# Kernel optimization log

Hardware: AMD Instinct MI355X
Metric: run time of the kernel (lower is better)

The kernel has to match this reference:

```python
import jax, jax.numpy as jnp
import numpy as np

N_NODES = 50000
N_EDGES = 800000
D_IN = 128
D_OUT = 128


def setup_inputs() -> dict:
    key = jax.random.key(0)
    k1, k2, k3, k4 = jax.random.split(key, 4)
    feature = jax.random.normal(k1, (N_NODES, D_IN), dtype=jnp.float32)
    edge_src = jax.random.randint(k2, (N_EDGES,), 0, N_NODES, dtype=jnp.int32)
    edge_dst = jax.random.randint(k3, (N_EDGES,), 0, N_NODES, dtype=jnp.int32)
    W = jax.random.normal(k4, (D_IN, D_OUT), dtype=jnp.float32) * (1.0 / np.sqrt(D_IN))
    b = jnp.zeros((D_OUT,), dtype=jnp.float32)
    return {"feature": feature, "edge_src": edge_src, "edge_dst": edge_dst, "W": W, "b": b}


def reference(feature, edge_src, edge_dst, W, b):
    # copy_src + sum reduce: for each edge, copy src node feature, sum into dst node
    msgs = feature[edge_src]  # [E, D_IN] gather
    h = jax.ops.segment_sum(msgs, edge_dst, num_segments=N_NODES)  # [N, D_IN]
    # linear + activation (relu)
    return jax.nn.relu(h @ W + b)
```

## Files before the change

kernel.cpp:

```cpp
#include <hip/hip_runtime.h>
#include <hip/hip_fp16.h>


constexpr int N    = 50000;
constexpr int E    = 800000;
constexpr int D    = 128;
constexpr int CAP  = 64;
constexpr int CSTR = 16;
constexpr int NT   = 3125;
constexpr int ZSTR = 136;
constexpr int SCB  = 391;

using f16x8 = __attribute__((ext_vector_type(8))) _Float16;
using f32x4 = __attribute__((ext_vector_type(4))) float;

__global__ void setup(const float* __restrict__ W, _Float16* __restrict__ Wf,
                      int* __restrict__ cnt) {
    const int tid = threadIdx.x;
    if (blockIdx.x < 8) {
        int t = blockIdx.x * 256 + tid;
        int ct = t >> 8, ks = (t >> 6) & 3, lane = t & 63;
        int q = lane >> 4, li = lane & 15;
        _Float16 v[8];
        #pragma unroll
        for (int j = 0; j < 8; ++j)
            v[j] = (_Float16)W[(ks * 32 + q * 8 + j) * D + ct * 16 + li];
        *(f16x8*)(Wf + (size_t)t * 8) = *(const f16x8*)v;
    } else {
        int i4 = (blockIdx.x - 8) * 256 + tid;
        if (i4 < N * CSTR / 4)
            ((int4*)cnt)[i4] = make_int4(0, 0, 0, 0);
    }
}

__global__ __launch_bounds__(256) void prep(
        const float* __restrict__ feature,
        const int*   __restrict__ esrc,
        const int*   __restrict__ edst,
        const _Float16* __restrict__ Wf,
        int* __restrict__ cnt,
        unsigned short* __restrict__ bucket,
        _Float16* __restrict__ Z) {
    const int tid = threadIdx.x;

    if (blockIdx.x < SCB) {
        const int t = blockIdx.x * 256 + tid;
        if (t * 8 >= E) return;
        const int e0 = t * 8;
        const int4 s0 = *(const int4*)(esrc + e0);
        const int4 s1 = *(const int4*)(esrc + e0 + 4);
        const int4 d0 = *(const int4*)(edst + e0);
        const int4 d1 = *(const int4*)(edst + e0 + 4);
        const int ds[8] = {d0.x, d0.y, d0.z, d0.w, d1.x, d1.y, d1.z, d1.w};
        const int ss[8] = {s0.x, s0.y, s0.z, s0.w, s1.x, s1.y, s1.z, s1.w};
        int ps[8];
        #pragma unroll
        for (int j = 0; j < 8; ++j)
            ps[j] = atomicAdd(&cnt[ds[j] * CSTR], 1);
        #pragma unroll
        for (int j = 0; j < 8; ++j)
            if (ps[j] < CAP)
                bucket[ds[j] * CAP + ps[j]] = (unsigned short)ss[j];
        return;
    }

    __shared__ _Float16 zs[4][16 * ZSTR];
    const int wave = tid >> 6, lane = tid & 63;
    const int wt = (blockIdx.x - SCB) * 4 + wave;
    if (wt >= NT) return;
    const int q = lane >> 4, li = lane & 15;

    const float* fp = feature + (size_t)(wt * 16 + li) * D + q * 8;
    f16x8 afr[4];
    #pragma unroll
    for (int ks = 0; ks < 4; ++ks) {
        const float4 u0 = *(const float4*)(fp + ks * 32);
        const float4 u1 = *(const float4*)(fp + ks * 32 + 4);
        afr[ks][0] = (_Float16)u0.x; afr[ks][1] = (_Float16)u0.y;
        afr[ks][2] = (_Float16)u0.z; afr[ks][3] = (_Float16)u0.w;
        afr[ks][4] = (_Float16)u1.x; afr[ks][5] = (_Float16)u1.y;
        afr[ks][6] = (_Float16)u1.z; afr[ks][7] = (_Float16)u1.w;
    }

    f32x4 acc[8];
    #pragma unroll
    for (int ct = 0; ct < 8; ++ct) acc[ct] = (f32x4){0.f, 0.f, 0.f, 0.f};
    #pragma unroll
    for (int ks = 0; ks < 4; ++ks)
        #pragma unroll
        for (int ct = 0; ct < 8; ++ct) {
            const f16x8 b = *(const f16x8*)(Wf + (size_t)((ct * 4 + ks) * 64 + lane) * 8);
            acc[ct] = __builtin_amdgcn_mfma_f32_16x16x32_f16(afr[ks], b, acc[ct], 0, 0, 0);
        }

    _Float16* zt = zs[wave];
    #pragma unroll
    for (int ct = 0; ct < 8; ++ct)
        #pragma unroll
        for (int r = 0; r < 4; ++r)
            zt[(q * 4 + r) * ZSTR + ct * 16 + li] = (_Float16)acc[ct][r];
    #pragma unroll
    for (int it = 0; it < 4; ++it) {
        const f16x8 v = *(const f16x8*)(zt + (it * 4 + q) * ZSTR + li * 8);
        *(f16x8*)(Z + (size_t)(wt * 16 + it * 4 + q) * D + li * 8) = v;
    }
}

__global__ __launch_bounds__(256) void gather(
        const _Float16* __restrict__ Z,
        const int* __restrict__ cnt,
        const unsigned short* __restrict__ bucket,
        const float* __restrict__ bias,
        float* __restrict__ out) {
    const int tid  = threadIdx.x;
    const int wave = tid >> 6, lane = tid & 63;
    const int g    = lane >> 4, li = lane & 15;
    const int nA   = blockIdx.x * 8 + wave * 2;
    const int nB   = nA + 1;

    const int degA = min(cnt[nA * CSTR], CAP);
    const int degB = min(cnt[nB * CSTR], CAP);
    const int srcA = bucket[nA * CAP + lane];
    const int srcB = bucket[nB * CAP + lane];
    const float4 b0 = *(const float4*)(bias + li * 8);
    const float4 b1 = *(const float4*)(bias + li * 8 + 4);

    float accA[8] = {0,0,0,0,0,0,0,0};
    float accB[8] = {0,0,0,0,0,0,0,0};

    const int mx = max(degA, degB);
    for (int base = 0; base < mx; base += 16) {
        f16x8 hA[4], hB[4];
        float mA[4], mB[4];
        #pragma unroll
        for (int t = 0; t < 4; ++t) {
            const int r  = base + t * 4 + g;
            const int sA = __shfl(srcA, min(r, max(degA - 1, 0)));
            const int sB = __shfl(srcB, min(r, max(degB - 1, 0)));
            mA[t] = (r < degA) ? 1.f : 0.f;
            mB[t] = (r < degB) ? 1.f : 0.f;
            hA[t] = *(const f16x8*)(Z + (size_t)sA * D + li * 8);
            hB[t] = *(const f16x8*)(Z + (size_t)sB * D + li * 8);
        }
        #pragma unroll
        for (int t = 0; t < 4; ++t)
            #pragma unroll
            for (int j = 0; j < 8; ++j) {
                accA[j] += mA[t] * (float)hA[t][j];
                accB[j] += mB[t] * (float)hB[t][j];
            }
    }

    #pragma unroll
    for (int j = 0; j < 8; ++j) {
        accA[j] += __shfl_xor(accA[j], 16);
        accA[j] += __shfl_xor(accA[j], 32);
        accB[j] += __shfl_xor(accB[j], 16);
        accB[j] += __shfl_xor(accB[j], 32);
    }

    if (g == 0) {
        float4 o0, o1;
        o0.x = fmaxf(accA[0] + b0.x, 0.f); o0.y = fmaxf(accA[1] + b0.y, 0.f);
        o0.z = fmaxf(accA[2] + b0.z, 0.f); o0.w = fmaxf(accA[3] + b0.w, 0.f);
        o1.x = fmaxf(accA[4] + b1.x, 0.f); o1.y = fmaxf(accA[5] + b1.y, 0.f);
        o1.z = fmaxf(accA[6] + b1.z, 0.f); o1.w = fmaxf(accA[7] + b1.w, 0.f);
        float* op = out + (size_t)nA * D + li * 8;
        *(float4*)op       = o0;
        *(float4*)(op + 4) = o1;
    } else if (g == 1) {
        float4 o0, o1;
        o0.x = fmaxf(accB[0] + b0.x, 0.f); o0.y = fmaxf(accB[1] + b0.y, 0.f);
        o0.z = fmaxf(accB[2] + b0.z, 0.f); o0.w = fmaxf(accB[3] + b0.w, 0.f);
        o1.x = fmaxf(accB[4] + b1.x, 0.f); o1.y = fmaxf(accB[5] + b1.y, 0.f);
        o1.z = fmaxf(accB[6] + b1.z, 0.f); o1.w = fmaxf(accB[7] + b1.w, 0.f);
        float* op = out + (size_t)nB * D + li * 8;
        *(float4*)op       = o0;
        *(float4*)(op + 4) = o1;
    }
}

extern "C" void kernel_launch(void* const* d_in, const int* in_sizes, int n_in,
                              void* d_out, int out_size, void* d_ws, size_t ws_size,
                              hipStream_t stream) {
    const float* feature = (const float*)d_in[0];
    const int*   esrc    = (const int*)d_in[1];
    const int*   edst    = (const int*)d_in[2];
    const float* W       = (const float*)d_in[3];
    const float* bias    = (const float*)d_in[4];
    float*       out     = (float*)d_out;

    int*            cnt    = (int*)d_ws;
    unsigned short* bucket = (unsigned short*)(cnt + (size_t)N * CSTR);
    _Float16*       Z      = (_Float16*)(bucket + (size_t)N * CAP);
    _Float16*       Wf     = Z + (size_t)N * D;

    setup<<<8 + (N * CSTR / 4 + 255) / 256, 256, 0, stream>>>(W, Wf, cnt);
    prep<<<SCB + (NT + 3) / 4, 256, 0, stream>>>(feature, esrc, edst, Wf, cnt, bucket, Z);
    gather<<<N / 8, 256, 0, stream>>>(Z, cnt, bucket, bias, out);
}
```

Before: 155.5 us.

## Replace global-atomic bucketing with two-level radix partition into per-node buckets

Edges are no longer bucketed by global atomics on padded per-node counters. A shared-memory histogram over 256-node ranges feeds a scan, a partition of edges into contiguous range segments, and a per-range kernel that builds node buckets with shared-memory atomics. This aims to remove contended scattered global atomics and the zeroing of a large padded counter array. It costs three extra kernel launches and an extra pass over the edge lists through an intermediate buffer.

```diff
diff --git a/kernel.cpp b/kernel.cpp
--- a/kernel.cpp
+++ b/kernel.cpp
@@ -6,67 +6,50 @@
 constexpr int E    = 800000;
 constexpr int D    = 128;
 constexpr int CAP  = 64;
-constexpr int CSTR = 16;
 constexpr int NT   = 3125;
 constexpr int ZSTR = 136;
-constexpr int SCB  = 391;
+constexpr int NR   = 196;
+constexpr int HB   = 256;
+constexpr int EPB  = E / HB;
 
 using f16x8 = __attribute__((ext_vector_type(8))) _Float16;
 using f32x4 = __attribute__((ext_vector_type(4))) float;
 
-__global__ void setup(const float* __restrict__ W, _Float16* __restrict__ Wf,
-                      int* __restrict__ cnt) {
-    const int tid = threadIdx.x;
-    if (blockIdx.x < 8) {
-        int t = blockIdx.x * 256 + tid;
-        int ct = t >> 8, ks = (t >> 6) & 3, lane = t & 63;
-        int q = lane >> 4, li = lane & 15;
-        _Float16 v[8];
-        #pragma unroll
-        for (int j = 0; j < 8; ++j)
-            v[j] = (_Float16)W[(ks * 32 + q * 8 + j) * D + ct * 16 + li];
-        *(f16x8*)(Wf + (size_t)t * 8) = *(const f16x8*)v;
-    } else {
-        int i4 = (blockIdx.x - 8) * 256 + tid;
-        if (i4 < N * CSTR / 4)
-            ((int4*)cnt)[i4] = make_int4(0, 0, 0, 0);
-    }
-}
-
-__global__ __launch_bounds__(256) void prep(
+__global__ void setup(const float* __restrict__ W, _Float16* __restrict__ Wf) {
+    int t = blockIdx.x * 256 + threadIdx.x;
+    int ct = t >> 8, ks = (t >> 6) & 3, lane = t & 63;
+    int q = lane >> 4, li = lane & 15;
+    _Float16 v[8];
+    #pragma unroll
+    for (int j = 0; j < 8; ++j)
+        v[j] = (_Float16)W[(ks * 32 + q * 8 + j) * D + ct * 16 + li];
+    *(f16x8*)(Wf + (size_t)t * 8) = *(const f16x8*)v;
+}
+
+__global__ __launch_bounds__(256) void midk(
         const float* __restrict__ feature,
-        const int*   __restrict__ esrc,
         const int*   __restrict__ edst,
         const _Float16* __restrict__ Wf,
-        int* __restrict__ cnt,
-        unsigned short* __restrict__ bucket,
+        int* __restrict__ hist,
         _Float16* __restrict__ Z) {
+    __shared__ int h[NR];
+    __shared__ _Float16 zs[4][16 * ZSTR];
     const int tid = threadIdx.x;
 
-    if (blockIdx.x < SCB) {
-        const int t = blockIdx.x * 256 + tid;
-        if (t * 8 >= E) return;
-        const int e0 = t * 8;
-        const int4 s0 = *(const int4*)(esrc + e0);
-        const int4 s1 = *(const int4*)(esrc + e0 + 4);
-        const int4 d0 = *(const int4*)(edst + e0);
-        const int4 d1 = *(const int4*)(edst + e0 + 4);
-        const int ds[8] = {d0.x, d0.y, d0.z, d0.w, d1.x, d1.y, d1.z, d1.w};
-        const int ss[8] = {s0.x, s0.y, s0.z, s0.w, s1.x, s1.y, s1.z, s1.w};
-        int ps[8];
-        #pragma unroll
-        for (int j = 0; j < 8; ++j)
-            ps[j] = atomicAdd(&cnt[ds[j] * CSTR], 1);
-        #pragma unroll
-        for (int j = 0; j < 8; ++j)
-            if (ps[j] < CAP)
-                bucket[ds[j] * CAP + ps[j]] = (unsigned short)ss[j];
+    if (blockIdx.x < HB) {
+        const int b = blockIdx.x;
+        if (tid < NR) h[tid] = 0;
+        __syncthreads();
+        const int e0 = b * EPB;
+        for (int i = tid; i < EPB; i += 256)
+            atomicAdd(&h[edst[e0 + i] >> 8], 1);
+        __syncthreads();
+        if (tid < NR) hist[b * NR + tid] = h[tid];
         return;
     }
 
-    __shared__ _Float16 zs[4][16 * ZSTR];
     const int wave = tid >> 6, lane = tid & 63;
-    const int wt = (blockIdx.x - SCB) * 4 + wave;
+    const int wt = (blockIdx.x - HB) * 4 + wave;
     if (wt >= NT) return;
     const int q = lane >> 4, li = lane & 15;
 
@@ -104,6 +87,97 @@
         const f16x8 v = *(const f16x8*)(zt + (it * 4 + q) * ZSTR + li * 8);
         *(f16x8*)(Z + (size_t)(wt * 16 + it * 4 + q) * D + li * 8) = v;
     }
+}
+
+__global__ void scank(int* __restrict__ hist, int* __restrict__ total) {
+    const int r    = blockIdx.x;
+    const int lane = threadIdx.x;
+    int h[4], sum = 0;
+    #pragma unroll
+    for (int j = 0; j < 4; ++j) {
+        h[j] = hist[(lane * 4 + j) * NR + r];
+        sum += h[j];
+    }
+    int incl = sum;
+    #pragma unroll
+    for (int off = 1; off < 64; off <<= 1) {
+        int u = __shfl_up(incl, off);
+        if (lane >= off) incl += u;
+    }
+    int run = incl - sum;
+    #pragma unroll
+    for (int j = 0; j < 4; ++j) {
+        hist[(lane * 4 + j) * NR + r] = run;
+        run += h[j];
+    }
+    if (lane == 63) total[r] = run;
+}
+
+__global__ __launch_bounds__(256) void partk(
+        const int* __restrict__ esrc,
+        const int* __restrict__ edst,
+        const int* __restrict__ blockBase,
+        const int* __restrict__ total,
+        int* __restrict__ rangeStartG,
+        unsigned int* __restrict__ part) {
+    __shared__ int rs[NR];
+    __shared__ int mb[NR];
+    __shared__ int rk[NR];
+    const int tid = threadIdx.x;
+    const int b   = blockIdx.x;
+
+    if (tid < 64) {
+        int carry = 0;
+        #pragma unroll
+        for (int c = 0; c < 4; ++c) {
+            int idx = c * 64 + tid;
+            int v = (idx < NR) ? total[idx] : 0;
+            int incl = v;
+            #pragma unroll
+            for (int off = 1; off < 64; off <<= 1) {
+                int u = __shfl_up(incl, off);
+                if (tid >= off) incl += u;
+            }
+            if (idx < NR) rs[idx] = incl - v + carry;
+            carry += __shfl(incl, 63);
+        }
+    }
+    if (tid < NR) { mb[tid] = blockBase[b * NR + tid]; rk[tid] = 0; }
+    __syncthreads();
+    if (b == 0 && tid < NR) rangeStartG[tid] = rs[tid];
+
+    const int e0 = b * EPB;
+    for (int i = tid; i < EPB; i += 256) {
+        const int s = esrc[e0 + i];
+        const int d = edst[e0 + i];
+        const int r = d >> 8;
+        const int k = atomicAdd(&rk[r], 1);
+        part[rs[r] + mb[r] + k] = ((unsigned)(d & 255) << 16) | (unsigned)s;
+    }
+}
+
+__global__ __launch_bounds__(256) void csrk(
+        const unsigned int* __restrict__ part,
+        const int* __restrict__ rangeStart,
+        const int* __restrict__ total,
+        unsigned short* __restrict__ bucket,
+        int* __restrict__ cnt) {
+    __shared__ int deg[256];
+    const int r = blockIdx.x, tid = threadIdx.x;
+    deg[tid] = 0;
+    __syncthreads();
+    const int rs = rangeStart[r], tot = total[r];
+    for (int i = tid; i < tot; i += 256) {
+        const unsigned p = part[rs + i];
+        const int local = p >> 16;
+        const int src   = p & 0xFFFF;
+        const int k = atomicAdd(&deg[local], 1);
+        if (k < CAP)
+            bucket[(((size_t)r << 8) + local) * CAP + k] = (unsigned short)src;
+    }
+    __syncthreads();
+    const int node = (r << 8) + tid;
+    if (node < N) cnt[node] = deg[tid];
 }
 
 __global__ __launch_bounds__(256) void gather(
@@ -118,8 +192,8 @@
     const int nA   = blockIdx.x * 8 + wave * 2;
     const int nB   = nA + 1;
 
-    const int degA = min(cnt[nA * CSTR], CAP);
-    const int degB = min(cnt[nB * CSTR], CAP);
+    const int degA = min(cnt[nA], CAP);
+    const int degB = min(cnt[nB], CAP);
     const int srcA = bucket[nA * CAP + lane];
     const int srcB = bucket[nB * CAP + lane];
     const float4 b0 = *(const float4*)(bias + li * 8);
@@ -191,11 +265,18 @@
     float*       out     = (float*)d_out;
 
     int*            cnt    = (int*)d_ws;
-    unsigned short* bucket = (unsigned short*)(cnt + (size_t)N * CSTR);
+    unsigned short* bucket = (unsigned short*)(cnt + N);
     _Float16*       Z      = (_Float16*)(bucket + (size_t)N * CAP);
     _Float16*       Wf     = Z + (size_t)N * D;
-
-    setup<<<8 + (N * CSTR / 4 + 255) / 256, 256, 0, stream>>>(W, Wf, cnt);
-    prep<<<SCB + (NT + 3) / 4, 256, 0, stream>>>(feature, esrc, edst, Wf, cnt, bucket, Z);
+    int*            hist   = (int*)(Wf + 16384);
+    int*            total  = hist + HB * NR;
+    int*            rangeS = total + NR;
+    unsigned int*   part   = (unsigned int*)(rangeS + NR);
+
+    setup<<<8, 256, 0, stream>>>(W, Wf);
+    midk <<<HB + (NT + 3) / 4, 256, 0, stream>>>(feature, edst, Wf, hist, Z);
+    scank<<<NR, 64, 0, stream>>>(hist, total);
+    partk<<<HB, 256, 0, stream>>>(esrc, edst, hist, total, rangeS, part);
+    csrk <<<NR, 256, 0, stream>>>(part, rangeS, total, bucket, cnt);
     gather<<<N / 8, 256, 0, stream>>>(Z, cnt, bucket, bias, out);
 }
```

New measurement: 152.0 us. 1.02x faster.
